# Kernel tuning notes

Measured on AMD Instinct MI355X. Metric: run time of the kernel, lower is better.

Reference implementation:

```python
import jax, jax.numpy as jnp
import numpy as np

NEG_INF = -1000000000.0


def _masked_softmax_scores(a, b, mask):
    # a: [B,H,S,D], b: [B,H,S,D] -> probs [B,H,S,S]
    d = a.shape[-1]
    scores = jnp.einsum('bhqd,bhkd->bhqk', a, b) / jnp.sqrt(jnp.asarray(d, a.dtype))
    scores = jnp.where(mask == 0, jnp.asarray(NEG_INF, scores.dtype), scores)
    return jax.nn.softmax(scores, axis=-1)


def setup_inputs() -> dict:
    key = jax.random.key(0)
    ks = jax.random.split(key, 8)
    B, H, S, D = 8, 12, 512, 64
    return {
        'query': jax.random.normal(ks[0], (B, H, S, D), dtype=jnp.float32),
        'key': jax.random.normal(ks[1], (B, H, S, D), dtype=jnp.float32),
        'value': jax.random.normal(ks[2], (B, H, S, D), dtype=jnp.float32),
        'mask': jax.random.randint(ks[3], (B, 1, S, S), 0, 2, dtype=jnp.int32),
        'x_original1': jax.random.normal(ks[4], (B, H, S, D), dtype=jnp.float32),
        'x_original2': jax.random.normal(ks[5], (B, H, S, D), dtype=jnp.float32),
        'x_position1': jax.random.normal(ks[6], (B, H, S, D), dtype=jnp.float32),
        'x_position2': jax.random.normal(ks[7], (B, H, S, D), dtype=jnp.float32),
    }


def reference(query, key, value, mask, x_original1, x_original2, x_position1, x_position2):
    p_attn = _masked_softmax_scores(query, key, mask)
    p_attn_ww = _masked_softmax_scores(x_original1, x_original2, mask)
    p_attn_wp = _masked_softmax_scores(x_original1, x_position2, mask)
    p_attn_pw = _masked_softmax_scores(x_position1, x_original2, mask)
    p_attn_pp = _masked_softmax_scores(x_position1, x_position2, mask)
    out = jnp.einsum('bhqk,bhkd->bhqd', p_attn, value)
    return (out, p_attn, p_attn_ww, p_attn_wp, p_attn_pw, p_attn_pp)
```

## Files before the change

### kernel.cpp

```cpp
#include <hip/hip_runtime.h>
#include <hip/hip_bf16.h>

typedef _Float16 f16;
typedef f16 f16x2 __attribute__((ext_vector_type(2)));
typedef f16 f16x4 __attribute__((ext_vector_type(4)));
typedef f16 f16x8 __attribute__((ext_vector_type(8)));
typedef float f32x4 __attribute__((ext_vector_type(4)));
typedef float f32x16 __attribute__((ext_vector_type(16)));

#define SEQ 512
#define DIM 64
#define NBH 96
#define OUT0 3145728
#define PSZ  25165824
#define MSZ  262144

__device__ __forceinline__ int swz(int row, int colByte) {
    return row * 128 + (colByte ^ ((row & 7) << 4));
}

__global__ __launch_bounds__(256) void scores_softmax(
    const float* __restrict__ q_, const float* __restrict__ k_,
    const float* __restrict__ xo1, const float* __restrict__ xo2,
    const float* __restrict__ xp1, const float* __restrict__ xp2,
    const int* __restrict__ mask, float* __restrict__ dout)
{
    __shared__ __align__(16) f16 As[32 * 64];
    __shared__ __align__(16) f16 Bs[128 * 64];
    __shared__ float red[4][32];

    const int tid = threadIdx.x;
    const int bid = blockIdx.x;
    const int qt  = bid & 15;
    const int bhm = bid >> 4;
    const int bh  = bhm % NBH;
    const int m   = bhm / NBH;

    const float* Ap; const float* Bp;
    if      (m == 0) { Ap = q_;  Bp = k_;  }
    else if (m == 1) { Ap = xo1; Bp = xo2; }
    else if (m == 2) { Ap = xo1; Bp = xp2; }
    else if (m == 3) { Ap = xp1; Bp = xo2; }
    else             { Ap = xp1; Bp = xp2; }

    const int w = tid >> 6, lane = tid & 63, l31 = lane & 31, half = lane >> 5;

    const float* Ag = Ap + ((size_t)bh * SEQ + qt * 32) * DIM;
#pragma unroll
    for (int i = 0; i < 2; i++) {
        int g = tid + 256 * i; int row = g >> 4, c4 = g & 15;
        f32x4 v = *reinterpret_cast<const f32x4*>(Ag + row * 64 + c4 * 4);
        f16x4 b; b[0]=(f16)v[0]; b[1]=(f16)v[1]; b[2]=(f16)v[2]; b[3]=(f16)v[3];
        *reinterpret_cast<f16x4*>((char*)As + swz(row, c4 * 8)) = b;
    }
    __syncthreads();

    f16x8 afr[4];
#pragma unroll
    for (int k4 = 0; k4 < 4; k4++)
        afr[k4] = *reinterpret_cast<const f16x8*>((char*)As + swz(l31, k4 * 32 + half * 16));

    f32x16 acc[4];
#pragma unroll
    for (int c = 0; c < 4; c++)
#pragma unroll
        for (int i = 0; i < 16; i++) acc[c][i] = 0.f;

    const float* Bg0 = Bp + (size_t)bh * SEQ * DIM;
    for (int c = 0; c < 4; c++) {
        __syncthreads();
        const float* Bg = Bg0 + (size_t)c * 128 * DIM;
#pragma unroll
        for (int i = 0; i < 8; i++) {
            int g = tid + 256 * i; int row = g >> 4, c4 = g & 15;
            f32x4 v = *reinterpret_cast<const f32x4*>(Bg + row * 64 + c4 * 4);
            f16x4 b; b[0]=(f16)v[0]; b[1]=(f16)v[1]; b[2]=(f16)v[2]; b[3]=(f16)v[3];
            *reinterpret_cast<f16x4*>((char*)Bs + swz(row, c4 * 8)) = b;
        }
        __syncthreads();
        int rb = w * 32 + l31;
#pragma unroll
        for (int k4 = 0; k4 < 4; k4++) {
            f16x8 bfr = *reinterpret_cast<const f16x8*>((char*)Bs + swz(rb, k4 * 32 + half * 16));
            acc[c] = __builtin_amdgcn_mfma_f32_32x32x16_f16(afr[k4], bfr, acc[c], 0, 0, 0);
        }
    }

    const int b = bh / 12;
    const int* mrow = mask + (size_t)b * MSZ + (size_t)(qt * 32) * SEQ;
    float rsum[16];
#pragma unroll
    for (int r = 0; r < 16; r++) rsum[r] = 0.f;
#pragma unroll
    for (int c = 0; c < 4; c++) {
        int kcol = c * 128 + w * 32 + l31;
#pragma unroll
        for (int r = 0; r < 16; r++) {
            int qrow = (r & 3) + 8 * (r >> 2) + 4 * half;
            int mk = mrow[(size_t)qrow * SEQ + kcol];
            float e = mk ? __expf(acc[c][r] * 0.125f) : 0.f;
            acc[c][r] = e;
            rsum[r] += e;
        }
    }
#pragma unroll
    for (int d = 1; d < 32; d <<= 1)
#pragma unroll
        for (int r = 0; r < 16; r++) rsum[r] += __shfl_xor(rsum[r], d);
    if (l31 == 0) {
#pragma unroll
        for (int r = 0; r < 16; r++) {
            int qrow = (r & 3) + 8 * (r >> 2) + 4 * half;
            red[w][qrow] = rsum[r];
        }
    }
    __syncthreads();
    float inv[16];
#pragma unroll
    for (int r = 0; r < 16; r++) {
        int qrow = (r & 3) + 8 * (r >> 2) + 4 * half;
        float s = red[0][qrow] + red[1][qrow] + red[2][qrow] + red[3][qrow];
        inv[r] = 1.0f / s;
    }
    float* P = dout + OUT0 + (size_t)m * PSZ + (size_t)bh * MSZ + (size_t)(qt * 32) * SEQ;
#pragma unroll
    for (int c = 0; c < 4; c++) {
        int kcol = c * 128 + w * 32 + l31;
#pragma unroll
        for (int r = 0; r < 16; r++) {
            int qrow = (r & 3) + 8 * (r >> 2) + 4 * half;
            P[(size_t)qrow * SEQ + kcol] = acc[c][r] * inv[r];
        }
    }
}

__global__ __launch_bounds__(256) void vtrans(const float* __restrict__ v, f16* __restrict__ vt)
{
    __shared__ float t[128][65];
    const int tid = threadIdx.x;
    const int bh = blockIdx.x >> 2, ck = blockIdx.x & 3;
    const float* Vg = v + ((size_t)bh * SEQ + ck * 128) * DIM;
#pragma unroll
    for (int i = 0; i < 8; i++) {
        int g = tid + 256 * i; int row = g >> 4, c4 = g & 15;
        f32x4 vv = *reinterpret_cast<const f32x4*>(Vg + row * 64 + c4 * 4);
        t[row][c4*4+0] = vv[0]; t[row][c4*4+1] = vv[1];
        t[row][c4*4+2] = vv[2]; t[row][c4*4+3] = vv[3];
    }
    __syncthreads();
    f16* Og = vt + (size_t)bh * DIM * SEQ + ck * 128;
#pragma unroll
    for (int i = 0; i < 16; i++) {
        int p = tid + 256 * i; int d = p >> 6; int j = (p & 63) * 2;
        f16x2 o; o[0] = (f16)t[j][d]; o[1] = (f16)t[j + 1][d];
        *reinterpret_cast<f16x2*>(Og + (size_t)d * SEQ + j) = o;
    }
}

__global__ __launch_bounds__(256) void pv_mfma(const float* __restrict__ dout,
                                               const f16* __restrict__ vt,
                                               float* __restrict__ out)
{
    __shared__ __align__(16) f16 Ps[64 * 64];
    __shared__ __align__(16) f16 Vs[64 * 64];
    const int tid = threadIdx.x;
    const int bh = blockIdx.x >> 3, qt = blockIdx.x & 7;
    const int w = tid >> 6, lane = tid & 63, l31 = lane & 31, half = lane >> 5;
    const int wr = w >> 1, wc = w & 1;

    const float* Pg = dout + OUT0 + (size_t)bh * MSZ + (size_t)(qt * 64) * SEQ;
    const f16* Vg = vt + (size_t)bh * DIM * SEQ;

    f32x16 acc;
#pragma unroll
    for (int i = 0; i < 16; i++) acc[i] = 0.f;

    for (int c = 0; c < 8; c++) {
        __syncthreads();
#pragma unroll
        for (int i = 0; i < 4; i++) {
            int g = tid + 256 * i; int row = g >> 4, c4 = g & 15;
            f32x4 v = *reinterpret_cast<const f32x4*>(Pg + (size_t)row * SEQ + c * 64 + c4 * 4);
            f16x4 b; b[0]=(f16)v[0]; b[1]=(f16)v[1]; b[2]=(f16)v[2]; b[3]=(f16)v[3];
            *reinterpret_cast<f16x4*>((char*)Ps + swz(row, c4 * 8)) = b;
        }
#pragma unroll
        for (int i = 0; i < 2; i++) {
            int g = tid + 256 * i; int row = g >> 3, c8 = g & 7;
            f16x8 v = *reinterpret_cast<const f16x8*>(Vg + (size_t)row * SEQ + c * 64 + c8 * 8);
            *reinterpret_cast<f16x8*>((char*)Vs + swz(row, c8 * 16)) = v;
        }
        __syncthreads();
        int qr = wr * 32 + l31, dr = wc * 32 + l31;
#pragma unroll
        for (int k4 = 0; k4 < 4; k4++) {
            int co = k4 * 32 + half * 16;
            f16x8 a  = *reinterpret_cast<const f16x8*>((char*)Ps + swz(qr, co));
            f16x8 bb = *reinterpret_cast<const f16x8*>((char*)Vs + swz(dr, co));
            acc = __builtin_amdgcn_mfma_f32_32x32x16_f16(a, bb, acc, 0, 0, 0);
        }
    }
    float* og = out + ((size_t)bh * SEQ + qt * 64 + wr * 32) * DIM + wc * 32;
#pragma unroll
    for (int r = 0; r < 16; r++) {
        int qrow = (r & 3) + 8 * (r >> 2) + 4 * half;
        og[(size_t)qrow * DIM + l31] = acc[r];
    }
}

__global__ __launch_bounds__(256) void pv_vec(const float* __restrict__ dout,
                                              const float* __restrict__ v,
                                              float* __restrict__ out)
{
    __shared__ float Vs[128][64];
    const int tid = threadIdx.x;
    const int bh = blockIdx.x >> 3, qt = blockIdx.x & 7;
    float accv[16];
#pragma unroll
    for (int j = 0; j < 16; j++) accv[j] = 0.f;
    const float* Prow = dout + OUT0 + ((size_t)bh * SEQ + qt * 64 + (tid >> 2)) * SEQ;
    const int dbase = (tid & 3) * 16;
    for (int ck = 0; ck < 4; ck++) {
        __syncthreads();
        const float* Vg = v + ((size_t)bh * SEQ + ck * 128) * DIM;
#pragma unroll
        for (int i = 0; i < 8; i++) {
            int g = tid + 256 * i; int row = g >> 4, c4 = g & 15;
            f32x4 vv = *reinterpret_cast<const f32x4*>(Vg + row * 64 + c4 * 4);
            Vs[row][c4*4+0] = vv[0]; Vs[row][c4*4+1] = vv[1];
            Vs[row][c4*4+2] = vv[2]; Vs[row][c4*4+3] = vv[3];
        }
        __syncthreads();
        for (int kv = 0; kv < 128; kv++) {
            float p = Prow[ck * 128 + kv];
#pragma unroll
            for (int j = 0; j < 16; j++) accv[j] += p * Vs[kv][dbase + j];
        }
    }
    float* og = out + ((size_t)bh * SEQ + qt * 64 + (tid >> 2)) * DIM + dbase;
#pragma unroll
    for (int j = 0; j < 16; j++) og[j] = accv[j];
}

extern "C" void kernel_launch(void* const* d_in, const int* in_sizes, int n_in,
                              void* d_out, int out_size, void* d_ws, size_t ws_size,
                              hipStream_t stream) {
    const float* q_  = (const float*)d_in[0];
    const float* k_  = (const float*)d_in[1];
    const float* v_  = (const float*)d_in[2];
    const int*   msk = (const int*)d_in[3];
    const float* xo1 = (const float*)d_in[4];
    const float* xo2 = (const float*)d_in[5];
    const float* xp1 = (const float*)d_in[6];
    const float* xp2 = (const float*)d_in[7];
    float* out = (float*)d_out;

    scores_softmax<<<5 * NBH * 16, 256, 0, stream>>>(q_, k_, xo1, xo2, xp1, xp2, msk, out);

    const size_t need = (size_t)NBH * DIM * SEQ * sizeof(f16);
    if (ws_size >= need) {
        f16* vt = (f16*)d_ws;
        vtrans<<<NBH * 4, 256, 0, stream>>>(v_, vt);
        pv_mfma<<<NBH * 8, 256, 0, stream>>>(out, vt, out);
    } else {
        pv_vec<<<NBH * 8, 256, 0, stream>>>(out, v_, out);
    }
}
```

Baseline: 713.6 us.

## Stage mask in shared memory as bytes, remap block order, use nontemporal P stores

The scores kernel now loads the 32x512 int32 mask tile with coalesced vector loads into shared memory as bytes at kernel start, replacing strided per-element global mask reads in the softmax loop. Block indices are remapped so consecutive blocks hit different batches, which changes which mask and input slices are resident in cache at the same time. Probability outputs are written with nontemporal stores and read back with nontemporal loads in the PV kernel, to avoid polluting cache with the large P arrays. This adds 16KB of LDS per block, which may lower occupancy.

Measured after the change: 688.8 us. 3.5% less time.

```diff
diff --git a/kernel.cpp b/kernel.cpp
--- a/kernel.cpp
+++ b/kernel.cpp
@@ -7,6 +7,9 @@
 typedef f16 f16x8 __attribute__((ext_vector_type(8)));
 typedef float f32x4 __attribute__((ext_vector_type(4)));
 typedef float f32x16 __attribute__((ext_vector_type(16)));
+typedef int i32x4 __attribute__((ext_vector_type(4)));
+typedef unsigned char u8;
+typedef u8 u8x4 __attribute__((ext_vector_type(4)));
 
 #define SEQ 512
 #define DIM 64
@@ -27,14 +30,18 @@
 {
     __shared__ __align__(16) f16 As[32 * 64];
     __shared__ __align__(16) f16 Bs[128 * 64];
+    __shared__ __align__(16) u8  Ms[32 * 512];
     __shared__ float red[4][32];
 
     const int tid = threadIdx.x;
     const int bid = blockIdx.x;
-    const int qt  = bid & 15;
-    const int bhm = bid >> 4;
-    const int bh  = bhm % NBH;
-    const int m   = bhm / NBH;
+    const int b   = bid & 7;
+    int t = bid >> 3;
+    const int qt = t & 15;
+    t >>= 4;
+    const int h  = t % 12;
+    const int m  = t / 12;
+    const int bh = b * 12 + h;
 
     const float* Ap; const float* Bp;
     if      (m == 0) { Ap = q_;  Bp = k_;  }
@@ -45,13 +52,24 @@
 
     const int w = tid >> 6, lane = tid & 63, l31 = lane & 31, half = lane >> 5;
 
+    const int* mrow = mask + (size_t)b * MSZ + (size_t)(qt * 32) * SEQ;
+#pragma unroll
+    for (int i = 0; i < 16; i++) {
+        int g = tid + 256 * i;
+        i32x4 mv = *reinterpret_cast<const i32x4*>(mrow + g * 4);
+        u8x4 pk;
+        pk[0] = (u8)(mv[0] != 0); pk[1] = (u8)(mv[1] != 0);
+        pk[2] = (u8)(mv[2] != 0); pk[3] = (u8)(mv[3] != 0);
+        *reinterpret_cast<u8x4*>(&Ms[g * 4]) = pk;
+    }
+
     const float* Ag = Ap + ((size_t)bh * SEQ + qt * 32) * DIM;
 #pragma unroll
     for (int i = 0; i < 2; i++) {
         int g = tid + 256 * i; int row = g >> 4, c4 = g & 15;
         f32x4 v = *reinterpret_cast<const f32x4*>(Ag + row * 64 + c4 * 4);
-        f16x4 b; b[0]=(f16)v[0]; b[1]=(f16)v[1]; b[2]=(f16)v[2]; b[3]=(f16)v[3];
-        *reinterpret_cast<f16x4*>((char*)As + swz(row, c4 * 8)) = b;
+        f16x4 bb; bb[0]=(f16)v[0]; bb[1]=(f16)v[1]; bb[2]=(f16)v[2]; bb[3]=(f16)v[3];
+        *reinterpret_cast<f16x4*>((char*)As + swz(row, c4 * 8)) = bb;
     }
     __syncthreads();
 
@@ -74,8 +92,8 @@
         for (int i = 0; i < 8; i++) {
             int g = tid + 256 * i; int row = g >> 4, c4 = g & 15;
             f32x4 v = *reinterpret_cast<const f32x4*>(Bg + row * 64 + c4 * 4);
-            f16x4 b; b[0]=(f16)v[0]; b[1]=(f16)v[1]; b[2]=(f16)v[2]; b[3]=(f16)v[3];
-            *reinterpret_cast<f16x4*>((char*)Bs + swz(row, c4 * 8)) = b;
+            f16x4 bb; bb[0]=(f16)v[0]; bb[1]=(f16)v[1]; bb[2]=(f16)v[2]; bb[3]=(f16)v[3];
+            *reinterpret_cast<f16x4*>((char*)Bs + swz(row, c4 * 8)) = bb;
         }
         __syncthreads();
         int rb = w * 32 + l31;
@@ -86,8 +104,6 @@
         }
     }
 
-    const int b = bh / 12;
-    const int* mrow = mask + (size_t)b * MSZ + (size_t)(qt * 32) * SEQ;
     float rsum[16];
 #pragma unroll
     for (int r = 0; r < 16; r++) rsum[r] = 0.f;
@@ -97,7 +113,7 @@
 #pragma unroll
         for (int r = 0; r < 16; r++) {
             int qrow = (r & 3) + 8 * (r >> 2) + 4 * half;
-            int mk = mrow[(size_t)qrow * SEQ + kcol];
+            int mk = Ms[qrow * 512 + kcol];
             float e = mk ? __expf(acc[c][r] * 0.125f) : 0.f;
             acc[c][r] = e;
             rsum[r] += e;
@@ -129,7 +145,7 @@
 #pragma unroll
         for (int r = 0; r < 16; r++) {
             int qrow = (r & 3) + 8 * (r >> 2) + 4 * half;
-            P[(size_t)qrow * SEQ + kcol] = acc[c][r] * inv[r];
+            __builtin_nontemporal_store(acc[c][r] * inv[r], &P[(size_t)qrow * SEQ + kcol]);
         }
     }
 }
@@ -138,7 +154,12 @@
 {
     __shared__ float t[128][65];
     const int tid = threadIdx.x;
-    const int bh = blockIdx.x >> 2, ck = blockIdx.x & 3;
+    const int bid = blockIdx.x;
+    const int b = bid & 7;
+    int r = bid >> 3;
+    const int ck = r & 3;
+    const int h  = r >> 2;
+    const int bh = b * 12 + h;
     const float* Vg = v + ((size_t)bh * SEQ + ck * 128) * DIM;
 #pragma unroll
     for (int i = 0; i < 8; i++) {
@@ -164,7 +185,12 @@
     __shared__ __align__(16) f16 Ps[64 * 64];
     __shared__ __align__(16) f16 Vs[64 * 64];
     const int tid = threadIdx.x;
-    const int bh = blockIdx.x >> 3, qt = blockIdx.x & 7;
+    const int bid = blockIdx.x;
+    const int b = bid & 7;
+    int r = bid >> 3;
+    const int qt = r & 7;
+    const int h  = r >> 3;
+    const int bh = b * 12 + h;
     const int w = tid >> 6, lane = tid & 63, l31 = lane & 31, half = lane >> 5;
     const int wr = w >> 1, wc = w & 1;
 
@@ -180,9 +206,10 @@
 #pragma unroll
         for (int i = 0; i < 4; i++) {
             int g = tid + 256 * i; int row = g >> 4, c4 = g & 15;
-            f32x4 v = *reinterpret_cast<const f32x4*>(Pg + (size_t)row * SEQ + c * 64 + c4 * 4);
-            f16x4 b; b[0]=(f16)v[0]; b[1]=(f16)v[1]; b[2]=(f16)v[2]; b[3]=(f16)v[3];
-            *reinterpret_cast<f16x4*>((char*)Ps + swz(row, c4 * 8)) = b;
+            f32x4 v = __builtin_nontemporal_load(
+                reinterpret_cast<const f32x4*>(Pg + (size_t)row * SEQ + c * 64 + c4 * 4));
+            f16x4 bb; bb[0]=(f16)v[0]; bb[1]=(f16)v[1]; bb[2]=(f16)v[2]; bb[3]=(f16)v[3];
+            *reinterpret_cast<f16x4*>((char*)Ps + swz(row, c4 * 8)) = bb;
         }
 #pragma unroll
         for (int i = 0; i < 2; i++) {
@@ -202,9 +229,9 @@
     }
     float* og = out + ((size_t)bh * SEQ + qt * 64 + wr * 32) * DIM + wc * 32;
 #pragma unroll
-    for (int r = 0; r < 16; r++) {
-        int qrow = (r & 3) + 8 * (r >> 2) + 4 * half;
-        og[(size_t)qrow * DIM + l31] = acc[r];
+    for (int r2 = 0; r2 < 16; r2++) {
+        int qrow = (r2 & 3) + 8 * (r2 >> 2) + 4 * half;
+        og[(size_t)qrow * DIM + l31] = acc[r2];
     }
 }
 
@@ -214,7 +241,12 @@
 {
     __shared__ float Vs[128][64];
     const int tid = threadIdx.x;
-    const int bh = blockIdx.x >> 3, qt = blockIdx.x & 7;
+    const int bid = blockIdx.x;
+    const int b = bid & 7;
+    int r = bid >> 3;
+    const int qt = r & 7;
+    const int h  = r >> 3;
+    const int bh = b * 12 + h;
     float accv[16];
 #pragma unroll
     for (int j = 0; j < 16; j++) accv[j] = 0.f;
```
